# Performance work log

Hardware: AMD Instinct MI355X
Metric: run time of the kernel (lower is better)

The kernel has to match this reference:

```python
import jax, jax.numpy as jnp
import numpy as np

B, H, S, D = 4, 16, 2048, 128
D_MODEL = 128  # scale factor per module init


def setup_inputs() -> dict:
    key = jax.random.key(0)
    kq, kk, kv = jax.random.split(key, 3)
    Q = jax.random.normal(kq, (B, H, S, D), dtype=jnp.float32)
    K = jax.random.normal(kk, (B, H, S, D), dtype=jnp.float32)
    V = jax.random.normal(kv, (B, H, S, D), dtype=jnp.float32)
    return {"Q": Q, "K": K, "V": V}


def reference(Q, K, V):
    # scores: [B, H, S, S]
    scores = jnp.einsum("bhqd,bhkd->bhqk", Q, K) / np.sqrt(D_MODEL).astype(np.float32)
    # causal mask: lower-triangular keeps, upper becomes -inf
    q_idx = jnp.arange(S)[:, None]
    k_idx = jnp.arange(S)[None, :]
    causal = q_idx >= k_idx  # [S, S]
    scores = jnp.where(causal, scores, -jnp.inf)
    attn = jax.nn.softmax(scores, axis=-1)
    return jnp.einsum("bhqk,bhkd->bhqd", attn, V)
```

## Files before the change

### kernel.cpp

```cpp
#include <hip/hip_runtime.h>

typedef _Float16 f16;
typedef _Float16 f16x4 __attribute__((ext_vector_type(4)));
typedef _Float16 f16x8 __attribute__((ext_vector_type(8)));
typedef float    f32x16 __attribute__((ext_vector_type(16)));
typedef int      i32x4 __attribute__((ext_vector_type(4)));

#define B_ 4
#define H_ 16
#define S_ 2048
#define D_ 128
#define KVB 32
#define KSTR 136
#define VTSTR 40

union U4 { i32x4 i; f16x8 h; };

__device__ __forceinline__ unsigned pk2(float a, float b) {
    auto v = __builtin_amdgcn_cvt_pkrtz(a, b);
    return __builtin_bit_cast(unsigned, v);
}

__device__ __forceinline__ f16x8 cvt8(const float4 a, const float4 b) {
    f16x8 h;
    h[0] = (f16)a.x; h[1] = (f16)a.y; h[2] = (f16)a.z; h[3] = (f16)a.w;
    h[4] = (f16)b.x; h[5] = (f16)b.y; h[6] = (f16)b.z; h[7] = (f16)b.w;
    return h;
}

__global__ __launch_bounds__(256)
void prep(const float* __restrict__ K, const float* __restrict__ V,
          const float* __restrict__ Q,
          f16* __restrict__ Kh, f16* __restrict__ Vtt, f16* __restrict__ Qh)
{
    const int bid = blockIdx.x;
    const int bh  = bid >> 5;
    const int kb  = bid & 31;
    const int k0  = kb * 64;
    const int tid = threadIdx.x;
    const float qmul = 0.08838834764831845f * 1.4426950408889634f;

    const float* Kb = K + ((size_t)bh * S_ + k0) * D_;
    const float* Vb = V + ((size_t)bh * S_ + k0) * D_;
    const float* Qb = Q + ((size_t)bh * S_ + k0) * D_;
    f16* Khb = Kh + ((size_t)bh * S_ + k0) * D_;
    f16* Qhb = Qh + ((size_t)bh * S_ + k0) * D_;
    f16* Vtb = Vtt + (size_t)bh * S_ * D_ + (size_t)kb * 2 * (D_ * 32);

    #pragma unroll
    for (int it = 0; it < 4; ++it) {
        const int idx = tid + it * 256;
        const int row = idx >> 4, c8 = idx & 15;
        const float4 a = *(const float4*)(Kb + row * D_ + c8 * 8);
        const float4 b = *(const float4*)(Kb + row * D_ + c8 * 8 + 4);
        *(f16x8*)(Khb + row * D_ + c8 * 8) = cvt8(a, b);
        float4 qa = *(const float4*)(Qb + row * D_ + c8 * 8);
        float4 qb = *(const float4*)(Qb + row * D_ + c8 * 8 + 4);
        qa.x *= qmul; qa.y *= qmul; qa.z *= qmul; qa.w *= qmul;
        qb.x *= qmul; qb.y *= qmul; qb.z *= qmul; qb.w *= qmul;
        *(f16x8*)(Qhb + row * D_ + c8 * 8) = cvt8(qa, qb);
    }
    #pragma unroll
    for (int it = 0; it < 4; ++it) {
        const int idx = tid + it * 256;
        const int d  = idx & 127;
        const int k8 = idx >> 7;
        const int t  = k8 >> 2;
        const int o  = k8 & 3;
        const int c  = o >> 1, odd = o & 1;
        const int kbase = t * 32 + c * 16 + odd * 4;
        const float* vp0 = Vb + (size_t)kbase * D_ + d;
        const float* vp1 = vp0 + (size_t)8 * D_;
        f16x8 vh;
        #pragma unroll
        for (int e = 0; e < 4; ++e) vh[e] = (f16)vp0[(size_t)e * D_];
        #pragma unroll
        for (int e = 0; e < 4; ++e) vh[4 + e] = (f16)vp1[(size_t)e * D_];
        *(f16x8*)(Vtb + (size_t)t * (D_ * 32) + d * 32 + o * 8) = vh;
    }
}

__global__ __launch_bounds__(256, 3)
void fattn17(const f16* __restrict__ Qhg, const f16* __restrict__ Khg,
             const f16* __restrict__ Vttg,
             f16* __restrict__ Pg, float2* __restrict__ mlg)
{
    __shared__ __align__(16) f16 Klds[2][KVB * KSTR];
    __shared__ __align__(16) f16 Vl[2][128 * VTSTR];

    const int id  = blockIdx.x;
    const int xcd = id & 7;
    const int r   = id >> 3;
    const int bh  = xcd + 8 * (r & 7);
    const int rr  = r >> 3;
    const int s   = rr & 1;
    const int qt  = 15 - (rr >> 1);

    const int tid  = threadIdx.x;
    const int lane = tid & 63;
    const int l31  = lane & 31;
    const int h    = lane >> 5;
    const int wv   = tid >> 6;

    const int qw0 = qt * 128 + wv * 32;
    const int qg  = qw0 + l31;

    const f16* Qhb = Qhg + (size_t)bh * S_ * D_;
    const f16* Khb = Khg + (size_t)bh * S_ * D_;
    const f16* Vtb = Vttg + (size_t)bh * S_ * D_;

    const int nkt  = 4 * qt + 4;
    const int half = 2 * qt + 2;
    const int lo   = s ? half : 0;
    const int hi   = s ? nkt : half;
    int lastt = 4 * qt + wv;
    if (lastt > hi - 1) lastt = hi - 1;

    const f16* kS = Khb + (tid >> 4) * D_ + (tid & 15) * 8;
    const f16* vS = Vtb + (size_t)tid * 8;
    const int  kDo = (tid >> 4) * KSTR + (tid & 15) * 8;
    const int  vDo = (tid >> 2) * VTSTR + (tid & 3) * 8;

    i32x4 kr[2], vr[2];
    auto issue = [&](int kt) {
        const f16* kp = kS + ((size_t)kt << 12);
        const f16* vp = vS + ((size_t)kt << 12);
        kr[0] = *(const i32x4*)kp;
        kr[1] = *(const i32x4*)(kp + 2048);
        vr[0] = *(const i32x4*)vp;
        vr[1] = *(const i32x4*)(vp + 2048);
    };
    auto writeLds = [&](int buf) {
        f16* kb = &Klds[buf][0];
        f16* vb = &Vl[buf][0];
        *(i32x4*)(kb + kDo)              = kr[0];
        *(i32x4*)(kb + kDo + 16 * KSTR)  = kr[1];
        *(i32x4*)(vb + vDo)              = vr[0];
        *(i32x4*)(vb + vDo + 64 * VTSTR) = vr[1];
    };

    f16x8 qf[8];
    {
        const f16* Qrow = Qhb + (size_t)(qw0 + l31) * D_;
        #pragma unroll
        for (int dc = 0; dc < 8; ++dc)
            qf[dc] = *(const f16x8*)(Qrow + dc * 16 + h * 8);
    }

    f32x16 acc[4];
    #pragma unroll
    for (int dt = 0; dt < 4; ++dt)
        #pragma unroll
        for (int q = 0; q < 16; ++q) acc[dt][q] = 0.f;
    float m_i = -1e30f, l_i = 0.f;

    issue(lo);
    writeLds(0);
    if (lo + 1 < hi) issue(lo + 1);
    __syncthreads();

    for (int kt = lo; kt < hi; ++kt) {
        const int cur = (kt - lo) & 1;

        if (kt <= lastt) {
            const int k0 = kt * KVB;
            f32x16 sv;
            #pragma unroll
            for (int q = 0; q < 16; ++q) sv[q] = 0.f;
            __builtin_amdgcn_s_setprio(1);
            #pragma unroll
            for (int dc = 0; dc < 8; ++dc) {
                const f16x8 kf = *(const f16x8*)&Klds[cur][l31 * KSTR + dc * 16 + h * 8];
                sv = __builtin_amdgcn_mfma_f32_32x32x16_f16(kf, qf[dc], sv, 0, 0, 0);
            }
            __builtin_amdgcn_s_setprio(0);
            if (k0 + 31 > qw0) {
                #pragma unroll
                for (int q = 0; q < 16; ++q) {
                    const int kg = k0 + (q & 3) + 8 * (q >> 2) + 4 * h;
                    if (kg > qg) sv[q] = -1e30f;
                }
            }
            const float a1 = fmaxf(fmaxf(sv[0], sv[1]), sv[2]);
            const float a2 = fmaxf(fmaxf(sv[3], sv[4]), sv[5]);
            const float a3 = fmaxf(fmaxf(sv[6], sv[7]), sv[8]);
            const float a4 = fmaxf(fmaxf(sv[9], sv[10]), sv[11]);
            const float a5 = fmaxf(fmaxf(sv[12], sv[13]), sv[14]);
            float mx = fmaxf(fmaxf(a1, a2), a3);
            mx = fmaxf(fmaxf(mx, a4), a5);
            mx = fmaxf(mx, sv[15]);
            mx = fmaxf(mx, __shfl_xor(mx, 32));
            if (!__all(mx - m_i <= 8.0f)) {
                const float mn = fmaxf(m_i, mx);
                const float al = exp2f(m_i - mn);
                m_i = mn;
                l_i *= al;
                float arow[16];
                #pragma unroll
                for (int q = 0; q < 16; ++q)
                    arow[q] = __shfl(al, (q & 3) + 8 * (q >> 2) + 4 * h);
                #pragma unroll
                for (int dt = 0; dt < 4; ++dt)
                    #pragma unroll
                    for (int q = 0; q < 16; ++q) acc[dt][q] *= arow[q];
            }
            #pragma unroll
            for (int q = 0; q < 16; ++q) sv[q] = exp2f(sv[q] - m_i);
            float s8[8];
            #pragma unroll
            for (int q = 0; q < 8; ++q) s8[q] = sv[2 * q] + sv[2 * q + 1];
            #pragma unroll
            for (int q = 0; q < 4; ++q) s8[q] += s8[q + 4];
            s8[0] += s8[2]; s8[1] += s8[3];
            float rsum = s8[0] + s8[1];
            rsum += __shfl_xor(rsum, 32);
            l_i += rsum;
            U4 pa0, pa1;
            #pragma unroll
            for (int m = 0; m < 4; ++m) {
                pa0.i[m] = (int)pk2(sv[2 * m],     sv[2 * m + 1]);
                pa1.i[m] = (int)pk2(sv[8 + 2 * m], sv[9 + 2 * m]);
            }
            __builtin_amdgcn_s_setprio(1);
            #pragma unroll
            for (int dt = 0; dt < 4; ++dt) {
                const f16* vrow = &Vl[cur][(dt * 32 + l31) * VTSTR + h * 8];
                const f16x8 b0 = *(const f16x8*)(vrow + 0);
                const f16x8 b1 = *(const f16x8*)(vrow + 16);
                acc[dt] = __builtin_amdgcn_mfma_f32_32x32x16_f16(pa0.h, b0, acc[dt], 0, 0, 0);
                acc[dt] = __builtin_amdgcn_mfma_f32_32x32x16_f16(pa1.h, b1, acc[dt], 0, 0, 0);
            }
            __builtin_amdgcn_s_setprio(0);
        }

        if (kt + 1 < hi) {
            writeLds(cur ^ 1);
            if (kt + 2 < hi) issue(kt + 2);
            __syncthreads();
        }
    }

    float li[16];
    #pragma unroll
    for (int q = 0; q < 16; ++q) {
        const float lv = __shfl(l_i, (q & 3) + 8 * (q >> 2) + 4 * h);
        li[q] = (lv > 0.f) ? 1.0f / lv : 0.f;
    }
    f16* Pb = Pg + ((size_t)s * (B_ * H_) + bh) * (S_ * D_);
    #pragma unroll
    for (int dt = 0; dt < 4; ++dt)
        #pragma unroll
        for (int q = 0; q < 16; ++q) {
            const int row = qw0 + (q & 3) + 8 * (q >> 2) + 4 * h;
            Pb[(size_t)row * D_ + dt * 32 + l31] = (f16)(acc[dt][q] * li[q]);
        }
    if (h == 0)
        mlg[((size_t)s * (B_ * H_) + bh) * S_ + qw0 + l31] = make_float2(m_i, l_i);
}

__global__ __launch_bounds__(256)
void merge(const f16* __restrict__ Pg, const float2* __restrict__ mlg,
           float* __restrict__ O)
{
    const size_t NROW   = (size_t)B_ * H_ * S_;
    const size_t total4 = NROW * (D_ / 4);
    const size_t stride = (size_t)gridDim.x * 256;
    for (size_t i = (size_t)blockIdx.x * 256 + threadIdx.x; i < total4; i += stride) {
        const size_t row = i >> 5;
        const float2 a = mlg[row];
        const float2 b = mlg[NROW + row];
        const float ms = fmaxf(a.x, b.x);
        float w0 = exp2f(a.x - ms) * a.y;
        float w1 = exp2f(b.x - ms) * b.y;
        const float inv = 1.0f / (w0 + w1);
        w0 *= inv; w1 *= inv;
        const f16x4 p0 = *(const f16x4*)(Pg + i * 4);
        const f16x4 p1 = *(const f16x4*)(Pg + NROW * D_ + i * 4);
        float4 o;
        o.x = w0 * (float)p0[0] + w1 * (float)p1[0];
        o.y = w0 * (float)p0[1] + w1 * (float)p1[1];
        o.z = w0 * (float)p0[2] + w1 * (float)p1[2];
        o.w = w0 * (float)p0[3] + w1 * (float)p1[3];
        *(float4*)(O + i * 4) = o;
    }
}

__global__ __launch_bounds__(256, 3)
void fattn5(const float* __restrict__ Qg, const float* __restrict__ Kg,
            const float* __restrict__ Vg, float* __restrict__ Og)
{
    __shared__ __align__(16) f16 Klds[2][KVB * KSTR];
    __shared__ __align__(16) f16 Vt[2][128 * VTSTR];
    const int id  = blockIdx.x;
    const int xcd = id & 7;
    const int w   = id >> 3;
    const int qt  = 15 - (w & 15);
    const int bh  = xcd + 8 * (w >> 4);
    const int tid  = threadIdx.x;
    const int lane = tid & 63;
    const int wv   = tid >> 6;
    const int l31  = lane & 31;
    const int h    = lane >> 5;
    const int qw0 = qt * 128 + wv * 32;
    const int qg  = qw0 + l31;
    const size_t base = (size_t)bh * S_ * D_;
    const float* Qb = Qg + base;
    const float* Kb = Kg + base;
    const float* Vb = Vg + base;
    float*       Ob = Og + base;
    const int nkt = 4 * qt + 4;
    float4 kr[4];
    float  vr[16];
    auto issue = [&](int kt) {
        const int k0n = kt * KVB;
        #pragma unroll
        for (int it = 0; it < 2; ++it) {
            const int idx  = tid + it * 256;
            const int krow = idx >> 4;
            const int c8   = idx & 15;
            const float* kp = Kb + (size_t)(k0n + krow) * D_ + c8 * 8;
            kr[it * 2]     = *(const float4*)kp;
            kr[it * 2 + 1] = *(const float4*)(kp + 4);
            const int d  = idx & 127;
            const int k8 = idx >> 7;
            const float* vp = Vb + (size_t)(k0n + k8 * 8) * D_ + d;
            #pragma unroll
            for (int e = 0; e < 8; ++e) vr[it * 8 + e] = vp[(size_t)e * D_];
        }
    };
    auto writeLds = [&](int buf) {
        #pragma unroll
        for (int it = 0; it < 2; ++it) {
            const int idx  = tid + it * 256;
            const int krow = idx >> 4;
            const int c8   = idx & 15;
            *(f16x8*)&Klds[buf][krow * KSTR + c8 * 8] = cvt8(kr[it * 2], kr[it * 2 + 1]);
            const int d  = idx & 127;
            const int k8 = idx >> 7;
            f16x8 vh;
            #pragma unroll
            for (int e = 0; e < 8; ++e) vh[e] = (f16)vr[it * 8 + e];
            *(f16x8*)&Vt[buf][d * VTSTR + k8 * 8] = vh;
        }
    };
    const float qmul = 0.08838834764831845f * 1.4426950408889634f;
    f16x8 qf[8];
    {
        const float* Qrow = Qb + (size_t)(qw0 + l31) * D_;
        #pragma unroll
        for (int dc = 0; dc < 8; ++dc) {
            const float4 a = *(const float4*)(Qrow + dc * 16 + h * 8);
            const float4 b = *(const float4*)(Qrow + dc * 16 + h * 8 + 4);
            f16x8 q;
            q[0] = (f16)(a.x * qmul); q[1] = (f16)(a.y * qmul);
            q[2] = (f16)(a.z * qmul); q[3] = (f16)(a.w * qmul);
            q[4] = (f16)(b.x * qmul); q[5] = (f16)(b.y * qmul);
            q[6] = (f16)(b.z * qmul); q[7] = (f16)(b.w * qmul);
            qf[dc] = q;
        }
    }
    f32x16 acc[4];
    #pragma unroll
    for (int dt = 0; dt < 4; ++dt)
        #pragma unroll
        for (int q = 0; q < 16; ++q) acc[dt][q] = 0.f;
    float m_i = -1e30f, l_i = 0.f;
    issue(0);
    writeLds(0);
    if (nkt > 1) issue(1);
    __syncthreads();
    for (int kt = 0; kt < nkt; ++kt) {
        const int k0  = kt * KVB;
        const int cur = kt & 1;
        if (k0 <= qw0 + 31) {
            f32x16 sv;
            #pragma unroll
            for (int q = 0; q < 16; ++q) sv[q] = 0.f;
            #pragma unroll
            for (int dc = 0; dc < 8; ++dc) {
                const f16x8 kf = *(const f16x8*)&Klds[cur][l31 * KSTR + dc * 16 + h * 8];
                sv = __builtin_amdgcn_mfma_f32_32x32x16_f16(kf, qf[dc], sv, 0, 0, 0);
            }
            if (k0 + 31 > qw0) {
                #pragma unroll
                for (int q = 0; q < 16; ++q) {
                    const int kg = k0 + (q & 3) + 8 * (q >> 2) + 4 * h;
                    if (kg > qg) sv[q] = -1e30f;
                }
            }
            float mx = sv[0];
            #pragma unroll
            for (int q = 1; q < 16; ++q) mx = fmaxf(mx, sv[q]);
            mx = fmaxf(mx, __shfl_xor(mx, 32));
            if (!__all(mx - m_i <= 8.0f)) {
                const float mn = fmaxf(m_i, mx);
                const float al = exp2f(m_i - mn);
                m_i = mn;
                l_i *= al;
                float arow[16];
                #pragma unroll
                for (int q = 0; q < 16; ++q)
                    arow[q] = __shfl(al, (q & 3) + 8 * (q >> 2) + 4 * h);
                #pragma unroll
                for (int dt = 0; dt < 4; ++dt)
                    #pragma unroll
                    for (int q = 0; q < 16; ++q) acc[dt][q] *= arow[q];
            }
            float rsum = 0.f;
            #pragma unroll
            for (int q = 0; q < 16; ++q) {
                sv[q] = exp2f(sv[q] - m_i);
                rsum += sv[q];
            }
            rsum += __shfl_xor(rsum, 32);
            l_i += rsum;
            U4 pa[2];
            {
                unsigned dwp[8];
                #pragma unroll
                for (int m = 0; m < 8; ++m) dwp[m] = pk2(sv[2 * m], sv[2 * m + 1]);
                #pragma unroll
                for (int hf = 0; hf < 2; ++hf) {
                    const unsigned a0 = dwp[hf * 4 + 0], a1 = dwp[hf * 4 + 1];
                    const unsigned b0 = dwp[hf * 4 + 2], b1 = dwp[hf * 4 + 3];
                    const unsigned sa0 = (unsigned)__shfl_xor((int)a0, 32);
                    const unsigned sa1 = (unsigned)__shfl_xor((int)a1, 32);
                    const unsigned sb0 = (unsigned)__shfl_xor((int)b0, 32);
                    const unsigned sb1 = (unsigned)__shfl_xor((int)b1, 32);
                    i32x4 d;
                    d[0] = h ? (int)sb0 : (int)a0;
                    d[1] = h ? (int)sb1 : (int)a1;
                    d[2] = h ? (int)b0  : (int)sa0;
                    d[3] = h ? (int)b1  : (int)sa1;
                    pa[hf].i = d;
                }
            }
            #pragma unroll
            for (int dt = 0; dt < 4; ++dt) {
                const f16* vrow = &Vt[cur][(dt * 32 + l31) * VTSTR + h * 8];
                const f16x8 vb0 = *(const f16x8*)(vrow + 0);
                const f16x8 vb1 = *(const f16x8*)(vrow + 16);
                acc[dt] = __builtin_amdgcn_mfma_f32_32x32x16_f16(pa[0].h, vb0, acc[dt], 0, 0, 0);
                acc[dt] = __builtin_amdgcn_mfma_f32_32x32x16_f16(pa[1].h, vb1, acc[dt], 0, 0, 0);
            }
        }
        if (kt + 1 < nkt) {
            writeLds(cur ^ 1);
            if (kt + 2 < nkt) issue(kt + 2);
            __syncthreads();
        }
    }
    float li[16];
    #pragma unroll
    for (int q = 0; q < 16; ++q) {
        const float lv = __shfl(l_i, (q & 3) + 8 * (q >> 2) + 4 * h);
        li[q] = 1.0f / lv;
    }
    #pragma unroll
    for (int dt = 0; dt < 4; ++dt)
        #pragma unroll
        for (int q = 0; q < 16; ++q) {
            const int row = qw0 + (q & 3) + 8 * (q >> 2) + 4 * h;
            Ob[(size_t)row * D_ + dt * 32 + l31] = acc[dt][q] * li[q];
        }
}

extern "C" void kernel_launch(void* const* d_in, const int* in_sizes, int n_in,
                              void* d_out, int out_size, void* d_ws, size_t ws_size,
                              hipStream_t stream) {
    (void)in_sizes; (void)n_in; (void)out_size;
    const float* Q = (const float*)d_in[0];
    const float* K = (const float*)d_in[1];
    const float* V = (const float*)d_in[2];
    float* O = (float*)d_out;
    const size_t elems = (size_t)B_ * H_ * S_ * D_;
    const size_t nrow  = (size_t)B_ * H_ * S_;
    const size_t need  = elems * 2 * 5 + nrow * sizeof(float2) * 2;
    if (ws_size >= need) {
        f16* Kh  = (f16*)d_ws;
        f16* Vtt = Kh + elems;
        f16* Qh  = Vtt + elems;
        f16* P   = Qh + elems;
        float2* ml = (float2*)(P + 2 * elems);
        prep<<<dim3(B_ * H_ * (S_ / 64)), dim3(256), 0, stream>>>(K, V, Q, Kh, Vtt, Qh);
        fattn17<<<dim3(2048), dim3(256), 0, stream>>>(Qh, Kh, Vtt, P, ml);
        merge<<<dim3(2048), dim3(256), 0, stream>>>(P, ml, O);
    } else {
        fattn5<<<dim3((S_ / 128) * B_ * H_), dim3(256), 0, stream>>>(Q, K, V, O);
    }
}
```

Before: 185.7 us.

## Replace split-KV plus merge with paired causal q-tile bins per block

Removes the two-way KV split, the fp16 partial output buffer and the merge kernel. Each block now processes one or two whole query tiles, pairing long and short causal tiles to balance work, and writes fp32 output directly. Q is read as fp32 and converted inside the attention kernel, with the softmax scale moved onto K during prep so Q no longer needs a prep pass. The cost is fewer blocks (704 instead of 2048), which gives less parallelism and a serial second phase in the paired blocks.

New measurement: 163.6 us. 1.14x faster.

```diff
diff --git a/kernel.cpp b/kernel.cpp
--- a/kernel.cpp
+++ b/kernel.cpp
@@ -1,7 +1,6 @@
 #include <hip/hip_runtime.h>
 
 typedef _Float16 f16;
-typedef _Float16 f16x4 __attribute__((ext_vector_type(4)));
 typedef _Float16 f16x8 __attribute__((ext_vector_type(8)));
 typedef float    f32x16 __attribute__((ext_vector_type(16)));
 typedef int      i32x4 __attribute__((ext_vector_type(4)));
@@ -30,8 +29,7 @@
 
 __global__ __launch_bounds__(256)
 void prep(const float* __restrict__ K, const float* __restrict__ V,
-          const float* __restrict__ Q,
-          f16* __restrict__ Kh, f16* __restrict__ Vtt, f16* __restrict__ Qh)
+          f16* __restrict__ Kh, f16* __restrict__ Vtt)
 {
     const int bid = blockIdx.x;
     const int bh  = bid >> 5;
@@ -42,23 +40,18 @@
 
     const float* Kb = K + ((size_t)bh * S_ + k0) * D_;
     const float* Vb = V + ((size_t)bh * S_ + k0) * D_;
-    const float* Qb = Q + ((size_t)bh * S_ + k0) * D_;
     f16* Khb = Kh + ((size_t)bh * S_ + k0) * D_;
-    f16* Qhb = Qh + ((size_t)bh * S_ + k0) * D_;
     f16* Vtb = Vtt + (size_t)bh * S_ * D_ + (size_t)kb * 2 * (D_ * 32);
 
     #pragma unroll
     for (int it = 0; it < 4; ++it) {
         const int idx = tid + it * 256;
         const int row = idx >> 4, c8 = idx & 15;
-        const float4 a = *(const float4*)(Kb + row * D_ + c8 * 8);
-        const float4 b = *(const float4*)(Kb + row * D_ + c8 * 8 + 4);
+        float4 a = *(const float4*)(Kb + row * D_ + c8 * 8);
+        float4 b = *(const float4*)(Kb + row * D_ + c8 * 8 + 4);
+        a.x *= qmul; a.y *= qmul; a.z *= qmul; a.w *= qmul;
+        b.x *= qmul; b.y *= qmul; b.z *= qmul; b.w *= qmul;
         *(f16x8*)(Khb + row * D_ + c8 * 8) = cvt8(a, b);
-        float4 qa = *(const float4*)(Qb + row * D_ + c8 * 8);
-        float4 qb = *(const float4*)(Qb + row * D_ + c8 * 8 + 4);
-        qa.x *= qmul; qa.y *= qmul; qa.z *= qmul; qa.w *= qmul;
-        qb.x *= qmul; qb.y *= qmul; qb.z *= qmul; qb.w *= qmul;
-        *(f16x8*)(Qhb + row * D_ + c8 * 8) = cvt8(qa, qb);
     }
     #pragma unroll
     for (int it = 0; it < 4; ++it) {
@@ -80,10 +73,12 @@
     }
 }
 
+__device__ __constant__ int QTA[11] = {15, 14, 13, 12, 11, 10, 9, 8, 7, 6, 5};
+__device__ __constant__ int QTB[11] = {-1, -1, -1, -1, -1, -1, 0, 1, 2, 3, 4};
+
 __global__ __launch_bounds__(256, 3)
-void fattn17(const f16* __restrict__ Qhg, const f16* __restrict__ Khg,
-             const f16* __restrict__ Vttg,
-             f16* __restrict__ Pg, float2* __restrict__ mlg)
+void fattn18(const float* __restrict__ Qg, const f16* __restrict__ Khg,
+             const f16* __restrict__ Vttg, float* __restrict__ Og)
 {
     __shared__ __align__(16) f16 Klds[2][KVB * KSTR];
     __shared__ __align__(16) f16 Vl[2][128 * VTSTR];
@@ -92,9 +87,7 @@
     const int xcd = id & 7;
     const int r   = id >> 3;
     const int bh  = xcd + 8 * (r & 7);
-    const int rr  = r >> 3;
-    const int s   = rr & 1;
-    const int qt  = 15 - (rr >> 1);
+    const int bin = r >> 3;
 
     const int tid  = threadIdx.x;
     const int lane = tid & 63;
@@ -102,19 +95,10 @@
     const int h    = lane >> 5;
     const int wv   = tid >> 6;
 
-    const int qw0 = qt * 128 + wv * 32;
-    const int qg  = qw0 + l31;
-
-    const f16* Qhb = Qhg + (size_t)bh * S_ * D_;
-    const f16* Khb = Khg + (size_t)bh * S_ * D_;
-    const f16* Vtb = Vttg + (size_t)bh * S_ * D_;
-
-    const int nkt  = 4 * qt + 4;
-    const int half = 2 * qt + 2;
-    const int lo   = s ? half : 0;
-    const int hi   = s ? nkt : half;
-    int lastt = 4 * qt + wv;
-    if (lastt > hi - 1) lastt = hi - 1;
+    const float* Qb  = Qg   + (size_t)bh * S_ * D_;
+    const f16*   Khb = Khg  + (size_t)bh * S_ * D_;
+    const f16*   Vtb = Vttg + (size_t)bh * S_ * D_;
+    float*       Ob  = Og   + (size_t)bh * S_ * D_;
 
     const f16* kS = Khb + (tid >> 4) * D_ + (tid & 15) * 8;
     const f16* vS = Vtb + (size_t)tid * 8;
@@ -139,149 +123,134 @@
         *(i32x4*)(vb + vDo + 64 * VTSTR) = vr[1];
     };
 
-    f16x8 qf[8];
-    {
-        const f16* Qrow = Qhb + (size_t)(qw0 + l31) * D_;
-        #pragma unroll
-        for (int dc = 0; dc < 8; ++dc)
-            qf[dc] = *(const f16x8*)(Qrow + dc * 16 + h * 8);
-    }
-
-    f32x16 acc[4];
-    #pragma unroll
-    for (int dt = 0; dt < 4; ++dt)
-        #pragma unroll
-        for (int q = 0; q < 16; ++q) acc[dt][q] = 0.f;
-    float m_i = -1e30f, l_i = 0.f;
-
-    issue(lo);
-    writeLds(0);
-    if (lo + 1 < hi) issue(lo + 1);
-    __syncthreads();
-
-    for (int kt = lo; kt < hi; ++kt) {
-        const int cur = (kt - lo) & 1;
-
-        if (kt <= lastt) {
-            const int k0 = kt * KVB;
-            f32x16 sv;
-            #pragma unroll
-            for (int q = 0; q < 16; ++q) sv[q] = 0.f;
-            __builtin_amdgcn_s_setprio(1);
+    const int nph = (QTB[bin] >= 0) ? 2 : 1;
+
+    #pragma unroll 1
+    for (int ph = 0; ph < nph; ++ph) {
+        const int qt  = ph ? QTB[bin] : QTA[bin];
+        const int qw0 = qt * 128 + wv * 32;
+        const int qg  = qw0 + l31;
+        const int nkt = 4 * qt + 4;
+        const int lastt = 4 * qt + wv;
+
+        f16x8 qf[8];
+        {
+            const float* Qrow = Qb + (size_t)(qw0 + l31) * D_;
             #pragma unroll
             for (int dc = 0; dc < 8; ++dc) {
-                const f16x8 kf = *(const f16x8*)&Klds[cur][l31 * KSTR + dc * 16 + h * 8];
-                sv = __builtin_amdgcn_mfma_f32_32x32x16_f16(kf, qf[dc], sv, 0, 0, 0);
-            }
-            __builtin_amdgcn_s_setprio(0);
-            if (k0 + 31 > qw0) {
-                #pragma unroll
-                for (int q = 0; q < 16; ++q) {
-                    const int kg = k0 + (q & 3) + 8 * (q >> 2) + 4 * h;
-                    if (kg > qg) sv[q] = -1e30f;
-                }
-            }
-            const float a1 = fmaxf(fmaxf(sv[0], sv[1]), sv[2]);
-            const float a2 = fmaxf(fmaxf(sv[3], sv[4]), sv[5]);
-            const float a3 = fmaxf(fmaxf(sv[6], sv[7]), sv[8]);
-            const float a4 = fmaxf(fmaxf(sv[9], sv[10]), sv[11]);
-            const float a5 = fmaxf(fmaxf(sv[12], sv[13]), sv[14]);
-            float mx = fmaxf(fmaxf(a1, a2), a3);
-            mx = fmaxf(fmaxf(mx, a4), a5);
-            mx = fmaxf(mx, sv[15]);
-            mx = fmaxf(mx, __shfl_xor(mx, 32));
-            if (!__all(mx - m_i <= 8.0f)) {
-                const float mn = fmaxf(m_i, mx);
-                const float al = exp2f(m_i - mn);
-                m_i = mn;
-                l_i *= al;
-                float arow[16];
-                #pragma unroll
-                for (int q = 0; q < 16; ++q)
-                    arow[q] = __shfl(al, (q & 3) + 8 * (q >> 2) + 4 * h);
-                #pragma unroll
-                for (int dt = 0; dt < 4; ++dt)
+                const float4 a = *(const float4*)(Qrow + dc * 16 + h * 8);
+                const float4 b = *(const float4*)(Qrow + dc * 16 + h * 8 + 4);
+                qf[dc] = cvt8(a, b);
+            }
+        }
+
+        f32x16 acc[4];
+        #pragma unroll
+        for (int dt = 0; dt < 4; ++dt)
+            #pragma unroll
+            for (int q = 0; q < 16; ++q) acc[dt][q] = 0.f;
+        float m_i = -1e30f, l_i = 0.f;
+
+        __syncthreads();
+        issue(0);
+        writeLds(0);
+        if (nkt > 1) issue(1);
+        __syncthreads();
+
+        for (int kt = 0; kt < nkt; ++kt) {
+            const int cur = kt & 1;
+
+            if (kt <= lastt) {
+                const int k0 = kt * KVB;
+                f32x16 sv;
+                #pragma unroll
+                for (int q = 0; q < 16; ++q) sv[q] = 0.f;
+                __builtin_amdgcn_s_setprio(1);
+                #pragma unroll
+                for (int dc = 0; dc < 8; ++dc) {
+                    const f16x8 kf = *(const f16x8*)&Klds[cur][l31 * KSTR + dc * 16 + h * 8];
+                    sv = __builtin_amdgcn_mfma_f32_32x32x16_f16(kf, qf[dc], sv, 0, 0, 0);
+                }
+                __builtin_amdgcn_s_setprio(0);
+                if (k0 + 31 > qw0) {
                     #pragma unroll
-                    for (int q = 0; q < 16; ++q) acc[dt][q] *= arow[q];
-            }
-            #pragma unroll
-            for (int q = 0; q < 16; ++q) sv[q] = exp2f(sv[q] - m_i);
-            float s8[8];
-            #pragma unroll
-            for (int q = 0; q < 8; ++q) s8[q] = sv[2 * q] + sv[2 * q + 1];
-            #pragma unroll
-            for (int q = 0; q < 4; ++q) s8[q] += s8[q + 4];
-            s8[0] += s8[2]; s8[1] += s8[3];
-            float rsum = s8[0] + s8[1];
-            rsum += __shfl_xor(rsum, 32);
-            l_i += rsum;
-            U4 pa0, pa1;
-            #pragma unroll
-            for (int m = 0; m < 4; ++m) {
-                pa0.i[m] = (int)pk2(sv[2 * m],     sv[2 * m + 1]);
-                pa1.i[m] = (int)pk2(sv[8 + 2 * m], sv[9 + 2 * m]);
-            }
-            __builtin_amdgcn_s_setprio(1);
-            #pragma unroll
-            for (int dt = 0; dt < 4; ++dt) {
-                const f16* vrow = &Vl[cur][(dt * 32 + l31) * VTSTR + h * 8];
-                const f16x8 b0 = *(const f16x8*)(vrow + 0);
-                const f16x8 b1 = *(const f16x8*)(vrow + 16);
-                acc[dt] = __builtin_amdgcn_mfma_f32_32x32x16_f16(pa0.h, b0, acc[dt], 0, 0, 0);
-                acc[dt] = __builtin_amdgcn_mfma_f32_32x32x16_f16(pa1.h, b1, acc[dt], 0, 0, 0);
-            }
-            __builtin_amdgcn_s_setprio(0);
-        }
-
-        if (kt + 1 < hi) {
-            writeLds(cur ^ 1);
-            if (kt + 2 < hi) issue(kt + 2);
-            __syncthreads();
-        }
-    }
-
-    float li[16];
-    #pragma unroll
-    for (int q = 0; q < 16; ++q) {
-        const float lv = __shfl(l_i, (q & 3) + 8 * (q >> 2) + 4 * h);
-        li[q] = (lv > 0.f) ? 1.0f / lv : 0.f;
-    }
-    f16* Pb = Pg + ((size_t)s * (B_ * H_) + bh) * (S_ * D_);
-    #pragma unroll
-    for (int dt = 0; dt < 4; ++dt)
+                    for (int q = 0; q < 16; ++q) {
+                        const int kg = k0 + (q & 3) + 8 * (q >> 2) + 4 * h;
+                        if (kg > qg) sv[q] = -1e30f;
+                    }
+                }
+                const float a1 = fmaxf(fmaxf(sv[0], sv[1]), sv[2]);
+                const float a2 = fmaxf(fmaxf(sv[3], sv[4]), sv[5]);
+                const float a3 = fmaxf(fmaxf(sv[6], sv[7]), sv[8]);
+                const float a4 = fmaxf(fmaxf(sv[9], sv[10]), sv[11]);
+                const float a5 = fmaxf(fmaxf(sv[12], sv[13]), sv[14]);
+                float mx = fmaxf(fmaxf(a1, a2), a3);
+                mx = fmaxf(fmaxf(mx, a4), a5);
+                mx = fmaxf(mx, sv[15]);
+                mx = fmaxf(mx, __shfl_xor(mx, 32));
+                if (!__all(mx - m_i <= 8.0f)) {
+                    const float mn = fmaxf(m_i, mx);
+                    const float al = exp2f(m_i - mn);
+                    m_i = mn;
+                    l_i *= al;
+                    float arow[16];
+                    #pragma unroll
+                    for (int q = 0; q < 16; ++q)
+                        arow[q] = __shfl(al, (q & 3) + 8 * (q >> 2) + 4 * h);
+                    #pragma unroll
+                    for (int dt = 0; dt < 4; ++dt)
+                        #pragma unroll
+                        for (int q = 0; q < 16; ++q) acc[dt][q] *= arow[q];
+                }
+                #pragma unroll
+                for (int q = 0; q < 16; ++q) sv[q] = exp2f(sv[q] - m_i);
+                float s8[8];
+                #pragma unroll
+                for (int q = 0; q < 8; ++q) s8[q] = sv[2 * q] + sv[2 * q + 1];
+                #pragma unroll
+                for (int q = 0; q < 4; ++q) s8[q] += s8[q + 4];
+                s8[0] += s8[2]; s8[1] += s8[3];
+                float rsum = s8[0] + s8[1];
+                rsum += __shfl_xor(rsum, 32);
+                l_i += rsum;
+                U4 pa0, pa1;
+                #pragma unroll
+                for (int m = 0; m < 4; ++m) {
+                    pa0.i[m] = (int)pk2(sv[2 * m],     sv[2 * m + 1]);
+                    pa1.i[m] = (int)pk2(sv[8 + 2 * m], sv[9 + 2 * m]);
+                }
+                __builtin_amdgcn_s_setprio(1);
+                #pragma unroll
+                for (int dt = 0; dt < 4; ++dt) {
+                    const f16* vrow = &Vl[cur][(dt * 32 + l31) * VTSTR + h * 8];
+                    const f16x8 b0 = *(const f16x8*)(vrow + 0);
+                    const f16x8 b1 = *(const f16x8*)(vrow + 16);
+                    acc[dt] = __builtin_amdgcn_mfma_f32_32x32x16_f16(pa0.h, b0, acc[dt], 0, 0, 0);
+                    acc[dt] = __builtin_amdgcn_mfma_f32_32x32x16_f16(pa1.h, b1, acc[dt], 0, 0, 0);
+                }
+                __builtin_amdgcn_s_setprio(0);
+            }
+
+            if (kt + 1 < nkt) {
+                writeLds(cur ^ 1);
+                if (kt + 2 < nkt) issue(kt + 2);
+                __syncthreads();
+            }
+        }
+
+        float li[16];
         #pragma unroll
         for (int q = 0; q < 16; ++q) {
-            const int row = qw0 + (q & 3) + 8 * (q >> 2) + 4 * h;
-            Pb[(size_t)row * D_ + dt * 32 + l31] = (f16)(acc[dt][q] * li[q]);
-        }
-    if (h == 0)
-        mlg[((size_t)s * (B_ * H_) + bh) * S_ + qw0 + l31] = make_float2(m_i, l_i);
-}
-
-__global__ __launch_bounds__(256)
-void merge(const f16* __restrict__ Pg, const float2* __restrict__ mlg,
-           float* __restrict__ O)
-{
-    const size_t NROW   = (size_t)B_ * H_ * S_;
-    const size_t total4 = NROW * (D_ / 4);
-    const size_t stride = (size_t)gridDim.x * 256;
-    for (size_t i = (size_t)blockIdx.x * 256 + threadIdx.x; i < total4; i += stride) {
-        const size_t row = i >> 5;
-        const float2 a = mlg[row];
-        const float2 b = mlg[NROW + row];
-        const float ms = fmaxf(a.x, b.x);
-        float w0 = exp2f(a.x - ms) * a.y;
-        float w1 = exp2f(b.x - ms) * b.y;
-        const float inv = 1.0f / (w0 + w1);
-        w0 *= inv; w1 *= inv;
-        const f16x4 p0 = *(const f16x4*)(Pg + i * 4);
-        const f16x4 p1 = *(const f16x4*)(Pg + NROW * D_ + i * 4);
-        float4 o;
-        o.x = w0 * (float)p0[0] + w1 * (float)p1[0];
-        o.y = w0 * (float)p0[1] + w1 * (float)p1[1];
-        o.z = w0 * (float)p0[2] + w1 * (float)p1[2];
-        o.w = w0 * (float)p0[3] + w1 * (float)p1[3];
-        *(float4*)(O + i * 4) = o;
+            const float lv = __shfl(l_i, (q & 3) + 8 * (q >> 2) + 4 * h);
+            li[q] = 1.0f / lv;
+        }
+        #pragma unroll
+        for (int dt = 0; dt < 4; ++dt)
+            #pragma unroll
+            for (int q = 0; q < 16; ++q) {
+                const int row = qw0 + (q & 3) + 8 * (q >> 2) + 4 * h;
+                Ob[(size_t)row * D_ + dt * 32 + l31] = acc[dt][q] * li[q];
+            }
     }
 }
 
@@ -473,18 +442,13 @@
     const float* K = (const float*)d_in[1];
     const float* V = (const float*)d_in[2];
     float* O = (float*)d_out;
-    const size_t elems = (size_t)B_ * H_ * S_ * D_;
-    const size_t nrow  = (size_t)B_ * H_ * S_;
-    const size_t need  = elems * 2 * 5 + nrow * sizeof(float2) * 2;
-    if (ws_size >= need) {
+    const size_t elems  = (size_t)B_ * H_ * S_ * D_;
+    const size_t needKV = elems * 2 * sizeof(f16);
+    if (ws_size >= needKV) {
         f16* Kh  = (f16*)d_ws;
         f16* Vtt = Kh + elems;
-        f16* Qh  = Vtt + elems;
-        f16* P   = Qh + elems;
-        float2* ml = (float2*)(P + 2 * elems);
-        prep<<<dim3(B_ * H_ * (S_ / 64)), dim3(256), 0, stream>>>(K, V, Q, Kh, Vtt, Qh);
-        fattn17<<<dim3(2048), dim3(256), 0, stream>>>(Qh, Kh, Vtt, P, ml);
-        merge<<<dim3(2048), dim3(256), 0, stream>>>(P, ml, O);
+        prep<<<dim3(B_ * H_ * (S_ / 64)), dim3(256), 0, stream>>>(K, V, Kh, Vtt);
+        fattn18<<<dim3(704), dim3(256), 0, stream>>>(Q, Kh, Vtt, O);
     } else {
         fattn5<<<dim3((S_ / 128) * B_ * H_), dim3(256), 0, stream>>>(Q, K, V, O);
     }
```

## Fold softmax scale into K and fuse split-merge into attention via completion counters

Applied to the files above, without the earlier changes.

The prep kernel stops converting Q and applies the softmax scale and log2e factor to K instead. The attention kernel reads fp32 Q directly and converts it to fp16 in registers. The separate merge kernel is removed: each attention block fences its partial output, bumps a per-(bh, q-tile) atomic counter, and the second block to arrive combines both halves into the final output. This saves the Q round trip through workspace and one kernel launch. In exchange it adds a memset of the counters, atomics and fences, and a tail merge inside the attention blocks.

Measured after the change: 634.6 us. 242% more time.

```diff
diff --git a/kernel.cpp b/kernel.cpp
--- a/kernel.cpp
+++ b/kernel.cpp
@@ -30,8 +30,7 @@
 
 __global__ __launch_bounds__(256)
 void prep(const float* __restrict__ K, const float* __restrict__ V,
-          const float* __restrict__ Q,
-          f16* __restrict__ Kh, f16* __restrict__ Vtt, f16* __restrict__ Qh)
+          f16* __restrict__ Kh, f16* __restrict__ Vtt)
 {
     const int bid = blockIdx.x;
     const int bh  = bid >> 5;
@@ -42,23 +41,18 @@
 
     const float* Kb = K + ((size_t)bh * S_ + k0) * D_;
     const float* Vb = V + ((size_t)bh * S_ + k0) * D_;
-    const float* Qb = Q + ((size_t)bh * S_ + k0) * D_;
     f16* Khb = Kh + ((size_t)bh * S_ + k0) * D_;
-    f16* Qhb = Qh + ((size_t)bh * S_ + k0) * D_;
     f16* Vtb = Vtt + (size_t)bh * S_ * D_ + (size_t)kb * 2 * (D_ * 32);
 
     #pragma unroll
     for (int it = 0; it < 4; ++it) {
         const int idx = tid + it * 256;
         const int row = idx >> 4, c8 = idx & 15;
-        const float4 a = *(const float4*)(Kb + row * D_ + c8 * 8);
-        const float4 b = *(const float4*)(Kb + row * D_ + c8 * 8 + 4);
+        float4 a = *(const float4*)(Kb + row * D_ + c8 * 8);
+        float4 b = *(const float4*)(Kb + row * D_ + c8 * 8 + 4);
+        a.x *= qmul; a.y *= qmul; a.z *= qmul; a.w *= qmul;
+        b.x *= qmul; b.y *= qmul; b.z *= qmul; b.w *= qmul;
         *(f16x8*)(Khb + row * D_ + c8 * 8) = cvt8(a, b);
-        float4 qa = *(const float4*)(Qb + row * D_ + c8 * 8);
-        float4 qb = *(const float4*)(Qb + row * D_ + c8 * 8 + 4);
-        qa.x *= qmul; qa.y *= qmul; qa.z *= qmul; qa.w *= qmul;
-        qb.x *= qmul; qb.y *= qmul; qb.z *= qmul; qb.w *= qmul;
-        *(f16x8*)(Qhb + row * D_ + c8 * 8) = cvt8(qa, qb);
     }
     #pragma unroll
     for (int it = 0; it < 4; ++it) {
@@ -81,12 +75,13 @@
 }
 
 __global__ __launch_bounds__(256, 3)
-void fattn17(const f16* __restrict__ Qhg, const f16* __restrict__ Khg,
-             const f16* __restrict__ Vttg,
-             f16* __restrict__ Pg, float2* __restrict__ mlg)
+void fattn19(const float* __restrict__ Qg, const f16* __restrict__ Khg,
+             const f16* __restrict__ Vttg, float* __restrict__ Og,
+             f16* __restrict__ Pg, float2* __restrict__ mlg, int* __restrict__ flags)
 {
     __shared__ __align__(16) f16 Klds[2][KVB * KSTR];
     __shared__ __align__(16) f16 Vl[2][128 * VTSTR];
+    __shared__ int oldv;
 
     const int id  = blockIdx.x;
     const int xcd = id & 7;
@@ -105,9 +100,9 @@
     const int qw0 = qt * 128 + wv * 32;
     const int qg  = qw0 + l31;
 
-    const f16* Qhb = Qhg + (size_t)bh * S_ * D_;
-    const f16* Khb = Khg + (size_t)bh * S_ * D_;
-    const f16* Vtb = Vttg + (size_t)bh * S_ * D_;
+    const float* Qb  = Qg  + (size_t)bh * S_ * D_;
+    const f16*   Khb = Khg + (size_t)bh * S_ * D_;
+    const f16*   Vtb = Vttg + (size_t)bh * S_ * D_;
 
     const int nkt  = 4 * qt + 4;
     const int half = 2 * qt + 2;
@@ -141,10 +136,13 @@
 
     f16x8 qf[8];
     {
-        const f16* Qrow = Qhb + (size_t)(qw0 + l31) * D_;
-        #pragma unroll
-        for (int dc = 0; dc < 8; ++dc)
-            qf[dc] = *(const f16x8*)(Qrow + dc * 16 + h * 8);
+        const float* Qrow = Qb + (size_t)(qw0 + l31) * D_;
+        #pragma unroll
+        for (int dc = 0; dc < 8; ++dc) {
+            const float4 a = *(const float4*)(Qrow + dc * 16 + h * 8);
+            const float4 b = *(const float4*)(Qrow + dc * 16 + h * 8 + 4);
+            qf[dc] = cvt8(a, b);
+        }
     }
 
     f32x16 acc[4];
@@ -256,32 +254,39 @@
         }
     if (h == 0)
         mlg[((size_t)s * (B_ * H_) + bh) * S_ + qw0 + l31] = make_float2(m_i, l_i);
-}
-
-__global__ __launch_bounds__(256)
-void merge(const f16* __restrict__ Pg, const float2* __restrict__ mlg,
-           float* __restrict__ O)
-{
-    const size_t NROW   = (size_t)B_ * H_ * S_;
-    const size_t total4 = NROW * (D_ / 4);
-    const size_t stride = (size_t)gridDim.x * 256;
-    for (size_t i = (size_t)blockIdx.x * 256 + threadIdx.x; i < total4; i += stride) {
-        const size_t row = i >> 5;
-        const float2 a = mlg[row];
-        const float2 b = mlg[NROW + row];
-        const float ms = fmaxf(a.x, b.x);
-        float w0 = exp2f(a.x - ms) * a.y;
-        float w1 = exp2f(b.x - ms) * b.y;
-        const float inv = 1.0f / (w0 + w1);
-        w0 *= inv; w1 *= inv;
-        const f16x4 p0 = *(const f16x4*)(Pg + i * 4);
-        const f16x4 p1 = *(const f16x4*)(Pg + NROW * D_ + i * 4);
-        float4 o;
-        o.x = w0 * (float)p0[0] + w1 * (float)p1[0];
-        o.y = w0 * (float)p0[1] + w1 * (float)p1[1];
-        o.z = w0 * (float)p0[2] + w1 * (float)p1[2];
-        o.w = w0 * (float)p0[3] + w1 * (float)p1[3];
-        *(float4*)(O + i * 4) = o;
+
+    __threadfence();
+    __syncthreads();
+    if (tid == 0) oldv = atomicAdd(&flags[bh * 16 + qt], 1);
+    __syncthreads();
+    if (oldv == 1) {
+        __threadfence();
+        const f16* P0 = Pg + (size_t)bh * (S_ * D_);
+        const f16* P1 = Pg + ((size_t)(B_ * H_) + bh) * (S_ * D_);
+        const float2* ml0 = mlg + (size_t)bh * S_;
+        const float2* ml1 = mlg + ((size_t)(B_ * H_) + bh) * S_;
+        float* Ob = Og + (size_t)bh * S_ * D_;
+        #pragma unroll
+        for (int it = 0; it < 16; ++it) {
+            const int i   = tid + it * 256;
+            const int row = qt * 128 + (i >> 5);
+            const int c4  = i & 31;
+            const float2 a = ml0[row];
+            const float2 b = ml1[row];
+            const float ms = fmaxf(a.x, b.x);
+            float w0 = exp2f(a.x - ms) * a.y;
+            float w1 = exp2f(b.x - ms) * b.y;
+            const float inv = 1.0f / (w0 + w1);
+            w0 *= inv; w1 *= inv;
+            const f16x4 p0 = *(const f16x4*)(P0 + (size_t)row * D_ + c4 * 4);
+            const f16x4 p1 = *(const f16x4*)(P1 + (size_t)row * D_ + c4 * 4);
+            float4 o;
+            o.x = w0 * (float)p0[0] + w1 * (float)p1[0];
+            o.y = w0 * (float)p0[1] + w1 * (float)p1[1];
+            o.z = w0 * (float)p0[2] + w1 * (float)p1[2];
+            o.w = w0 * (float)p0[3] + w1 * (float)p1[3];
+            *(float4*)(Ob + (size_t)row * D_ + c4 * 4) = o;
+        }
     }
 }
 
@@ -475,16 +480,18 @@
     float* O = (float*)d_out;
     const size_t elems = (size_t)B_ * H_ * S_ * D_;
     const size_t nrow  = (size_t)B_ * H_ * S_;
-    const size_t need  = elems * 2 * 5 + nrow * sizeof(float2) * 2;
+    const size_t need  = elems * 2 * 4
+                       + nrow * 2 * sizeof(float2)
+                       + 1024 * sizeof(int);
     if (ws_size >= need) {
         f16* Kh  = (f16*)d_ws;
         f16* Vtt = Kh + elems;
-        f16* Qh  = Vtt + elems;
-        f16* P   = Qh + elems;
+        f16* P   = Vtt + elems;
         float2* ml = (float2*)(P + 2 * elems);
-        prep<<<dim3(B_ * H_ * (S_ / 64)), dim3(256), 0, stream>>>(K, V, Q, Kh, Vtt, Qh);
-        fattn17<<<dim3(2048), dim3(256), 0, stream>>>(Qh, Kh, Vtt, P, ml);
-        merge<<<dim3(2048), dim3(256), 0, stream>>>(P, ml, O);
+        int* flags = (int*)(ml + 2 * nrow);
+        hipMemsetAsync(flags, 0, 1024 * sizeof(int), stream);
+        prep<<<dim3(B_ * H_ * (S_ / 64)), dim3(256), 0, stream>>>(K, V, Kh, Vtt);
+        fattn19<<<dim3(2048), dim3(256), 0, stream>>>(Q, Kh, Vtt, O, P, ml, flags);
     } else {
         fattn5<<<dim3((S_ / 128) * B_ * H_), dim3(256), 0, stream>>>(Q, K, V, O);
     }
```
